# Performance work log

Hardware: AMD Instinct MI355X
Metric: run time of the kernel (lower is better)

The kernel has to match this reference:

```python
import jax, jax.numpy as jnp
import numpy as np

B, CIN, X, Y, Z = 4, 1, 64, 64, 64
W = 32          # fno_layer_size
L = 6           # num_fno_layers
M = 32          # modes per axis
CLIFT = CIN + 3 # coord features appended


def setup_inputs() -> dict:
    key = jax.random.key(0)
    ks = jax.random.split(key, 16)
    scale = 1.0 / (W * W)
    inp = {
        "x": jax.random.normal(ks[0], (B, CIN, X, Y, Z), dtype=jnp.float32),
        # lift network (two 1x1 conv3d layers)
        "lw1": jax.random.normal(ks[1], (W // 2, CLIFT), dtype=jnp.float32) * 0.1,
        "lb1": jnp.zeros((W // 2,), dtype=jnp.float32),
        "lw2": jax.random.normal(ks[2], (W, W // 2), dtype=jnp.float32) * 0.1,
        "lb2": jnp.zeros((W,), dtype=jnp.float32),
        # factorized spectral weights per layer: [L, in, out, modes, 2]
        "wx": jax.random.uniform(ks[3], (L, W, W, M, 2), dtype=jnp.float32) * scale,
        "wy": jax.random.uniform(ks[4], (L, W, W, M, 2), dtype=jnp.float32) * scale,
        "wz": jax.random.uniform(ks[5], (L, W, W, M, 2), dtype=jnp.float32) * scale,
        # per-layer MLP (1x1 conv3d: W -> 2W -> W)
        "mw1": jax.random.normal(ks[6], (L, 2 * W, W), dtype=jnp.float32) * 0.1,
        "mb1": jnp.zeros((L, 2 * W), dtype=jnp.float32),
        "mw2": jax.random.normal(ks[7], (L, W, 2 * W), dtype=jnp.float32) * 0.1,
        "mb2": jnp.zeros((L, W), dtype=jnp.float32),
    }
    return inp


def _pw(x, w, b):
    # 1x1x1 conv3d == per-voxel channel matmul
    return jnp.einsum('bixyz,oi->boxyz', x, w) + b[None, :, None, None, None]


def _spectral(x, wx, wy, wz):
    # x: [B, C, X, Y, Z]; wx/wy/wz: [C, C, M, 2] real -> complex
    cx = wx[..., 0] + 1j * wx[..., 1]
    cy = wy[..., 0] + 1j * wy[..., 1]
    cz = wz[..., 0] + 1j * wz[..., 1]
    _, _, sx, sy, sz = x.shape
    # z axis
    xf = jnp.fft.rfft(x, axis=-1, norm='ortho')
    oz = jnp.einsum('bixyz,ioz->boxyz', xf[..., :M], cz)
    oz = jnp.pad(oz, [(0, 0)] * 4 + [(0, sz // 2 + 1 - M)])
    out = jnp.fft.irfft(oz, n=sz, axis=-1, norm='ortho')
    # y axis
    xf = jnp.fft.rfft(x, axis=-2, norm='ortho')
    oy = jnp.einsum('bixyz,ioy->boxyz', xf[:, :, :, :M, :], cy)
    oy = jnp.pad(oy, [(0, 0)] * 3 + [(0, sy // 2 + 1 - M), (0, 0)])
    out = out + jnp.fft.irfft(oy, n=sy, axis=-2, norm='ortho')
    # x axis
    xf = jnp.fft.rfft(x, axis=-3, norm='ortho')
    ox = jnp.einsum('bixyz,iox->boxyz', xf[:, :, :M, :, :], cx)
    ox = jnp.pad(ox, [(0, 0)] * 2 + [(0, sx // 2 + 1 - M), (0, 0), (0, 0)])
    out = out + jnp.fft.irfft(ox, n=sx, axis=-3, norm='ortho')
    return out


def _meshgrid(b, sx, sy, sz, dtype):
    gx = jnp.linspace(0.0, 1.0, sx, dtype=dtype)
    gy = jnp.linspace(0.0, 1.0, sy, dtype=dtype)
    gz = jnp.linspace(0.0, 1.0, sz, dtype=dtype)
    GX, GY, GZ = jnp.meshgrid(gx, gy, gz, indexing='ij')
    g = jnp.stack([GX, GY, GZ], axis=0)            # [3, X, Y, Z]
    return jnp.broadcast_to(g[None], (b, 3, sx, sy, sz))


def reference(x, lw1, lb1, lw2, lb2, wx, wy, wz, mw1, mb1, mw2, mb2):
    b = x.shape[0]
    coord = _meshgrid(b, X, Y, Z, x.dtype)
    h = jnp.concatenate([x, coord], axis=1)         # [B, CIN+3, X, Y, Z]
    h = _pw(h, lw1, lb1)
    h = jax.nn.gelu(h, approximate=False)
    h = _pw(h, lw2, lb2)
    for l in range(L):
        s = _spectral(h, wx[l], wy[l], wz[l])
        s = _pw(s, mw1[l], mb1[l])
        s = jax.nn.gelu(s, approximate=False)
        s = _pw(s, mw2[l], mb2[l])
        h = s + h
    return h
```

## Files before the change

kernel.cpp:

```cpp
#include <hip/hip_runtime.h>
#include <math.h>


#define BB 4
#define CC 32
#define NN 64
#define MM 32
#define NSITE 8
#define STH 512

__global__ __launch_bounds__(256) void lift_kernel(
    const float* __restrict__ x,
    const float* __restrict__ lw1, const float* __restrict__ lb1,
    const float* __restrict__ lw2, const float* __restrict__ lb2,
    float* __restrict__ h)
{
    __shared__ float w1[64], b1s[16], w2[512], b2s[32];
    int tid = threadIdx.x;
    if (tid < 64) w1[tid] = lw1[tid];
    if (tid < 16) b1s[tid] = lb1[tid];
    for (int i = tid; i < 512; i += 256) w2[i] = lw2[i];
    if (tid < 32) b2s[tid] = lb2[tid];
    __syncthreads();

    int v = blockIdx.x * 256 + tid;
    int b = v >> 18;
    int vox = v & 262143;
    float feat0 = x[b * 262144 + vox];
    float feat1 = (float)(vox >> 12)        * (1.0f / 63.0f);
    float feat2 = (float)((vox >> 6) & 63)  * (1.0f / 63.0f);
    float feat3 = (float)(vox & 63)         * (1.0f / 63.0f);

    float t1[16];
#pragma unroll
    for (int o = 0; o < 16; ++o) {
        float a = b1s[o];
        a = fmaf(w1[o * 4 + 0], feat0, a);
        a = fmaf(w1[o * 4 + 1], feat1, a);
        a = fmaf(w1[o * 4 + 2], feat2, a);
        a = fmaf(w1[o * 4 + 3], feat3, a);
        t1[o] = 0.5f * a * (1.0f + erff(a * 0.70710678118654752f));
    }
    int base = b * CC * 262144 + vox;
#pragma unroll
    for (int c = 0; c < 32; ++c) {
        float a = b2s[c];
#pragma unroll
        for (int o = 0; o < 16; ++o) a = fmaf(w2[c * 16 + o], t1[o], a);
        h[base + c * 262144] = a;
    }
}

template <int AXIS, bool ACCUM>
__global__ __launch_bounds__(STH) void spectral_kernel(
    const float* __restrict__ h, float* __restrict__ sout,
    const float2* __restrict__ w)
{
    __shared__ float lds[34176];
    float*  xm    = lds;
    float2* mspec = (float2*)lds;
    float2* spec  = (float2*)(lds + 16896);
    float*  ybuf  = lds + 16896;
    float2* roots = (float2*)(lds + 34048);

    const int tid = threadIdx.x;
    const int site0 = blockIdx.x * NSITE;
    const int b  = site0 >> 12;
    const int q0 = site0 & 4095;

    if (tid < 64) {
        float ss, sc;
        sincosf((float)tid * (6.283185307179586f / 64.0f), &ss, &sc);
        roots[tid] = make_float2(sc, ss);
    }
    __syncthreads();

#pragma unroll
    for (int k = 0; k < 32; ++k) {
        int e = tid + k * STH;
        int c, s, t;
        if (AXIS == 2) { t = e & 63; s = (e >> 6) & 7; c = e >> 9; }
        else           { s = e & 7;  t = (e >> 3) & 63; c = e >> 9; }
        int q = q0 + s;
        int addr;
        if (AXIS == 2)      addr = (b * CC + c) * 262144 + q * 64 + t;
        else if (AXIS == 1) addr = (b * CC + c) * 262144 + (q >> 6) * 4096 + t * 64 + (q & 63);
        else                addr = (b * CC + c) * 262144 + t * 4096 + (q >> 6) * 64 + (q & 63);
        xm[(c * NSITE + s) * 66 + t] = h[addr];
    }
    __syncthreads();

    {
        const int mt = tid & 7;
        const int lt = tid >> 3;
        const int m0 = mt * 4;
        float ar[4][4], ai[4][4];
#pragma unroll
        for (int j = 0; j < 4; ++j)
#pragma unroll
            for (int i = 0; i < 4; ++i) { ar[j][i] = 0.0f; ai[j][i] = 0.0f; }
        int idx0 = 0, idx1 = 0, idx2 = 0, idx3 = 0;
        for (int t = 0; t < 64; ++t) {
            float xv[4];
#pragma unroll
            for (int j = 0; j < 4; ++j) xv[j] = xm[(lt * 4 + j) * 66 + t];
            float2 r0 = roots[idx0], r1 = roots[idx1], r2 = roots[idx2], r3 = roots[idx3];
            idx0 = (idx0 + m0 + 0) & 63;
            idx1 = (idx1 + m0 + 1) & 63;
            idx2 = (idx2 + m0 + 2) & 63;
            idx3 = (idx3 + m0 + 3) & 63;
#pragma unroll
            for (int j = 0; j < 4; ++j) {
                ar[j][0] = fmaf(xv[j], r0.x, ar[j][0]); ai[j][0] = fmaf(-xv[j], r0.y, ai[j][0]);
                ar[j][1] = fmaf(xv[j], r1.x, ar[j][1]); ai[j][1] = fmaf(-xv[j], r1.y, ai[j][1]);
                ar[j][2] = fmaf(xv[j], r2.x, ar[j][2]); ai[j][2] = fmaf(-xv[j], r2.y, ai[j][2]);
                ar[j][3] = fmaf(xv[j], r3.x, ar[j][3]); ai[j][3] = fmaf(-xv[j], r3.y, ai[j][3]);
            }
        }
#pragma unroll
        for (int j = 0; j < 4; ++j) {
            int line = lt * 4 + j;
            int c = line >> 3, s = line & 7;
#pragma unroll
            for (int i = 0; i < 4; ++i)
                spec[(s * CC + c) * MM + m0 + i] =
                    make_float2(ar[j][i] * 0.125f, ai[j][i] * 0.125f);
        }
    }
    __syncthreads();

    {
        const int m  = tid & 31;
        const int st = (tid >> 5) & 1;
        const int ot = tid >> 6;
        float ar[4][4], ai[4][4];
#pragma unroll
        for (int js = 0; js < 4; ++js)
#pragma unroll
            for (int jo = 0; jo < 4; ++jo) { ar[js][jo] = 0.0f; ai[js][jo] = 0.0f; }
        for (int i = 0; i < CC; ++i) {
            float2 sv[4];
#pragma unroll
            for (int js = 0; js < 4; ++js) sv[js] = spec[((st * 4 + js) * CC + i) * MM + m];
#pragma unroll
            for (int jo = 0; jo < 4; ++jo) {
                float2 wv = w[(i * CC + ot * 4 + jo) * MM + m];
#pragma unroll
                for (int js = 0; js < 4; ++js) {
                    ar[js][jo] = fmaf(sv[js].x, wv.x, fmaf(-sv[js].y, wv.y, ar[js][jo]));
                    ai[js][jo] = fmaf(sv[js].x, wv.y, fmaf( sv[js].y, wv.x, ai[js][jo]));
                }
            }
        }
        __syncthreads();
#pragma unroll
        for (int js = 0; js < 4; ++js) {
            int s = st * 4 + js;
#pragma unroll
            for (int jo = 0; jo < 4; ++jo) {
                int o = ot * 4 + jo;
                mspec[(o * NSITE + s) * 33 + m] = make_float2(ar[js][jo], ai[js][jo]);
            }
        }
    }
    __syncthreads();

    {
        const int tt = tid & 7;
        const int lt = tid >> 3;
        float acc[4][8];
#pragma unroll
        for (int j = 0; j < 4; ++j) {
            float m0r = mspec[(lt * 4 + j) * 33].x;
#pragma unroll
            for (int u = 0; u < 8; ++u) acc[j][u] = 0.5f * m0r;
        }
        for (int m = 1; m < 32; ++m) {
            float2 sv[4];
#pragma unroll
            for (int j = 0; j < 4; ++j) sv[j] = mspec[(lt * 4 + j) * 33 + m];
            int idx = (m * tt * 8) & 63;
#pragma unroll
            for (int u = 0; u < 8; ++u) {
                float2 rt = roots[idx];
                idx = (idx + m) & 63;
#pragma unroll
                for (int j = 0; j < 4; ++j) {
                    acc[j][u] = fmaf(sv[j].x, rt.x, acc[j][u]);
                    acc[j][u] = fmaf(-sv[j].y, rt.y, acc[j][u]);
                }
            }
        }
#pragma unroll
        for (int j = 0; j < 4; ++j)
#pragma unroll
            for (int u = 0; u < 8; ++u)
                ybuf[(lt * 4 + j) * 67 + tt * 8 + u] = acc[j][u] * 0.25f;
    }
    __syncthreads();

#pragma unroll
    for (int k = 0; k < 32; ++k) {
        int e = tid + k * STH;
        int o, s, t;
        if (AXIS == 2) { t = e & 63; s = (e >> 6) & 7; o = e >> 9; }
        else           { s = e & 7;  t = (e >> 3) & 63; o = e >> 9; }
        int q = q0 + s;
        int addr;
        if (AXIS == 2)      addr = (b * CC + o) * 262144 + q * 64 + t;
        else if (AXIS == 1) addr = (b * CC + o) * 262144 + (q >> 6) * 4096 + t * 64 + (q & 63);
        else                addr = (b * CC + o) * 262144 + t * 4096 + (q >> 6) * 64 + (q & 63);
        float v = ybuf[(o * NSITE + s) * 67 + t];
        if (ACCUM) sout[addr] += v;
        else       sout[addr] = v;
    }
}

__global__ __launch_bounds__(256) void mlp_kernel(
    const float* __restrict__ sin_, float* hio,
    const float* __restrict__ mw1, const float* __restrict__ mb1,
    const float* __restrict__ mw2, const float* __restrict__ mb2)
{
    __shared__ float w1[2048], bb1[64], w2[2048], bb2[32];
    int tid = threadIdx.x;
    for (int i = tid; i < 2048; i += 256) { w1[i] = mw1[i]; w2[i] = mw2[i]; }
    if (tid < 64) bb1[tid] = mb1[tid];
    if (tid < 32) bb2[tid] = mb2[tid];
    __syncthreads();

    int v = blockIdx.x * 256 + tid;
    int b = v >> 18;
    int vox = v & 262143;
    int base = b * CC * 262144 + vox;

    float sv[32];
#pragma unroll
    for (int i = 0; i < 32; ++i) sv[i] = sin_[base + i * 262144];

    float t1[64];
#pragma unroll
    for (int o = 0; o < 64; ++o) {
        float a = bb1[o];
#pragma unroll
        for (int i = 0; i < 32; ++i) a = fmaf(w1[o * 32 + i], sv[i], a);
        t1[o] = 0.5f * a * (1.0f + erff(a * 0.70710678118654752f));
    }
#pragma unroll
    for (int c = 0; c < 32; ++c) {
        float a = bb2[c];
#pragma unroll
        for (int o = 0; o < 64; ++o) a = fmaf(w2[c * 64 + o], t1[o], a);
        hio[base + c * 262144] += a;
    }
}

extern "C" void kernel_launch(void* const* d_in, const int* in_sizes, int n_in,
                              void* d_out, int out_size, void* d_ws, size_t ws_size,
                              hipStream_t stream) {
    const float* x   = (const float*)d_in[0];
    const float* lw1 = (const float*)d_in[1];
    const float* lb1 = (const float*)d_in[2];
    const float* lw2 = (const float*)d_in[3];
    const float* lb2 = (const float*)d_in[4];
    const float* wx  = (const float*)d_in[5];
    const float* wy  = (const float*)d_in[6];
    const float* wz  = (const float*)d_in[7];
    const float* mw1 = (const float*)d_in[8];
    const float* mb1 = (const float*)d_in[9];
    const float* mw2 = (const float*)d_in[10];
    const float* mb2 = (const float*)d_in[11];

    float* h = (float*)d_out;
    float* s = (float*)d_ws;

    lift_kernel<<<4096, 256, 0, stream>>>(x, lw1, lb1, lw2, lb2, h);

    for (int l = 0; l < 6; ++l) {
        const float2* wxl = (const float2*)wx + l * 32768;
        const float2* wyl = (const float2*)wy + l * 32768;
        const float2* wzl = (const float2*)wz + l * 32768;
        spectral_kernel<2, false><<<2048, STH, 0, stream>>>(h, s, wzl);
        spectral_kernel<1, true ><<<2048, STH, 0, stream>>>(h, s, wyl);
        spectral_kernel<0, true ><<<2048, STH, 0, stream>>>(h, s, wxl);
        mlp_kernel<<<4096, 256, 0, stream>>>(s, h,
            mw1 + l * 2048, mb1 + l * 64, mw2 + l * 2048, mb2 + l * 32);
    }
}
```

Before: 9.702 ms.

## Halve spectral sites per block and restructure MLP for fewer live registers

The spectral kernel now handles 4 lines per block instead of 8. This halves its LDS footprint and per-thread accumulator arrays and doubles the grid, with a launch-bounds hint asking for 4 blocks per CU, so more blocks fit on each CU. The MLP kernel no longer holds a 64-wide hidden vector in registers. It processes the hidden layer in chunks of 16 and accumulates outputs directly, reading a transposed second weight matrix from LDS as float4. The trade-off is less reuse per block in the spectral stages, since each thread covers fewer lines per twiddle or weight load, and possible spills if the register bounds are too tight.

Measured after the change: 32.23 ms. 3.32x slower.

```diff
diff --git a/kernel.cpp b/kernel.cpp
--- a/kernel.cpp
+++ b/kernel.cpp
@@ -6,7 +6,7 @@
 #define CC 32
 #define NN 64
 #define MM 32
-#define NSITE 8
+#define NSITE 4
 #define STH 512
 
 __global__ __launch_bounds__(256) void lift_kernel(
@@ -52,16 +52,16 @@
 }
 
 template <int AXIS, bool ACCUM>
-__global__ __launch_bounds__(STH) void spectral_kernel(
+__global__ __launch_bounds__(STH, 4) void spectral_kernel(
     const float* __restrict__ h, float* __restrict__ sout,
     const float2* __restrict__ w)
 {
-    __shared__ float lds[34176];
+    __shared__ float lds[17152];
     float*  xm    = lds;
     float2* mspec = (float2*)lds;
-    float2* spec  = (float2*)(lds + 16896);
-    float*  ybuf  = lds + 16896;
-    float2* roots = (float2*)(lds + 34048);
+    float2* spec  = (float2*)(lds + 8448);
+    float*  ybuf  = lds + 8448;
+    float2* roots = (float2*)(lds + 17024);
 
     const int tid = threadIdx.x;
     const int site0 = blockIdx.x * NSITE;
@@ -73,14 +73,13 @@
         sincosf((float)tid * (6.283185307179586f / 64.0f), &ss, &sc);
         roots[tid] = make_float2(sc, ss);
     }
-    __syncthreads();
-
-#pragma unroll
-    for (int k = 0; k < 32; ++k) {
+
+#pragma unroll
+    for (int k = 0; k < 16; ++k) {
         int e = tid + k * STH;
         int c, s, t;
-        if (AXIS == 2) { t = e & 63; s = (e >> 6) & 7; c = e >> 9; }
-        else           { s = e & 7;  t = (e >> 3) & 63; c = e >> 9; }
+        if (AXIS == 2) { t = e & 63; s = (e >> 6) & 3; c = e >> 8; }
+        else           { s = e & 3;  t = (e >> 2) & 63; c = e >> 8; }
         int q = q0 + s;
         int addr;
         if (AXIS == 2)      addr = (b * CC + c) * 262144 + q * 64 + t;
@@ -94,23 +93,23 @@
         const int mt = tid & 7;
         const int lt = tid >> 3;
         const int m0 = mt * 4;
-        float ar[4][4], ai[4][4];
-#pragma unroll
-        for (int j = 0; j < 4; ++j)
+        float ar[2][4], ai[2][4];
+#pragma unroll
+        for (int j = 0; j < 2; ++j)
 #pragma unroll
             for (int i = 0; i < 4; ++i) { ar[j][i] = 0.0f; ai[j][i] = 0.0f; }
         int idx0 = 0, idx1 = 0, idx2 = 0, idx3 = 0;
         for (int t = 0; t < 64; ++t) {
-            float xv[4];
-#pragma unroll
-            for (int j = 0; j < 4; ++j) xv[j] = xm[(lt * 4 + j) * 66 + t];
+            float xv[2];
+#pragma unroll
+            for (int j = 0; j < 2; ++j) xv[j] = xm[(lt * 2 + j) * 66 + t];
             float2 r0 = roots[idx0], r1 = roots[idx1], r2 = roots[idx2], r3 = roots[idx3];
             idx0 = (idx0 + m0 + 0) & 63;
             idx1 = (idx1 + m0 + 1) & 63;
             idx2 = (idx2 + m0 + 2) & 63;
             idx3 = (idx3 + m0 + 3) & 63;
 #pragma unroll
-            for (int j = 0; j < 4; ++j) {
+            for (int j = 0; j < 2; ++j) {
                 ar[j][0] = fmaf(xv[j], r0.x, ar[j][0]); ai[j][0] = fmaf(-xv[j], r0.y, ai[j][0]);
                 ar[j][1] = fmaf(xv[j], r1.x, ar[j][1]); ai[j][1] = fmaf(-xv[j], r1.y, ai[j][1]);
                 ar[j][2] = fmaf(xv[j], r2.x, ar[j][2]); ai[j][2] = fmaf(-xv[j], r2.y, ai[j][2]);
@@ -118,9 +117,9 @@
             }
         }
 #pragma unroll
-        for (int j = 0; j < 4; ++j) {
-            int line = lt * 4 + j;
-            int c = line >> 3, s = line & 7;
+        for (int j = 0; j < 2; ++j) {
+            int line = lt * 2 + j;
+            int c = line >> 2, s = line & 3;
 #pragma unroll
             for (int i = 0; i < 4; ++i)
                 spec[(s * CC + c) * MM + m0 + i] =
@@ -131,22 +130,22 @@
 
     {
         const int m  = tid & 31;
-        const int st = (tid >> 5) & 1;
+        const int sp = (tid >> 5) & 1;
         const int ot = tid >> 6;
-        float ar[4][4], ai[4][4];
-#pragma unroll
-        for (int js = 0; js < 4; ++js)
+        float ar[2][4], ai[2][4];
+#pragma unroll
+        for (int js = 0; js < 2; ++js)
 #pragma unroll
             for (int jo = 0; jo < 4; ++jo) { ar[js][jo] = 0.0f; ai[js][jo] = 0.0f; }
         for (int i = 0; i < CC; ++i) {
-            float2 sv[4];
-#pragma unroll
-            for (int js = 0; js < 4; ++js) sv[js] = spec[((st * 4 + js) * CC + i) * MM + m];
+            float2 sv[2];
+#pragma unroll
+            for (int js = 0; js < 2; ++js) sv[js] = spec[((sp * 2 + js) * CC + i) * MM + m];
 #pragma unroll
             for (int jo = 0; jo < 4; ++jo) {
                 float2 wv = w[(i * CC + ot * 4 + jo) * MM + m];
 #pragma unroll
-                for (int js = 0; js < 4; ++js) {
+                for (int js = 0; js < 2; ++js) {
                     ar[js][jo] = fmaf(sv[js].x, wv.x, fmaf(-sv[js].y, wv.y, ar[js][jo]));
                     ai[js][jo] = fmaf(sv[js].x, wv.y, fmaf( sv[js].y, wv.x, ai[js][jo]));
                 }
@@ -154,8 +153,8 @@
         }
         __syncthreads();
 #pragma unroll
-        for (int js = 0; js < 4; ++js) {
-            int s = st * 4 + js;
+        for (int js = 0; js < 2; ++js) {
+            int s = sp * 2 + js;
 #pragma unroll
             for (int jo = 0; jo < 4; ++jo) {
                 int o = ot * 4 + jo;
@@ -168,43 +167,43 @@
     {
         const int tt = tid & 7;
         const int lt = tid >> 3;
-        float acc[4][8];
-#pragma unroll
-        for (int j = 0; j < 4; ++j) {
-            float m0r = mspec[(lt * 4 + j) * 33].x;
+        float acc[2][8];
+#pragma unroll
+        for (int j = 0; j < 2; ++j) {
+            float m0r = mspec[(lt * 2 + j) * 33].x;
 #pragma unroll
             for (int u = 0; u < 8; ++u) acc[j][u] = 0.5f * m0r;
         }
         for (int m = 1; m < 32; ++m) {
-            float2 sv[4];
-#pragma unroll
-            for (int j = 0; j < 4; ++j) sv[j] = mspec[(lt * 4 + j) * 33 + m];
+            float2 sv[2];
+#pragma unroll
+            for (int j = 0; j < 2; ++j) sv[j] = mspec[(lt * 2 + j) * 33 + m];
             int idx = (m * tt * 8) & 63;
 #pragma unroll
             for (int u = 0; u < 8; ++u) {
                 float2 rt = roots[idx];
                 idx = (idx + m) & 63;
 #pragma unroll
-                for (int j = 0; j < 4; ++j) {
+                for (int j = 0; j < 2; ++j) {
                     acc[j][u] = fmaf(sv[j].x, rt.x, acc[j][u]);
                     acc[j][u] = fmaf(-sv[j].y, rt.y, acc[j][u]);
                 }
             }
         }
 #pragma unroll
-        for (int j = 0; j < 4; ++j)
+        for (int j = 0; j < 2; ++j)
 #pragma unroll
             for (int u = 0; u < 8; ++u)
-                ybuf[(lt * 4 + j) * 67 + tt * 8 + u] = acc[j][u] * 0.25f;
-    }
-    __syncthreads();
-
-#pragma unroll
-    for (int k = 0; k < 32; ++k) {
+                ybuf[(lt * 2 + j) * 67 + tt * 8 + u] = acc[j][u] * 0.25f;
+    }
+    __syncthreads();
+
+#pragma unroll
+    for (int k = 0; k < 16; ++k) {
         int e = tid + k * STH;
         int o, s, t;
-        if (AXIS == 2) { t = e & 63; s = (e >> 6) & 7; o = e >> 9; }
-        else           { s = e & 7;  t = (e >> 3) & 63; o = e >> 9; }
+        if (AXIS == 2) { t = e & 63; s = (e >> 6) & 3; o = e >> 8; }
+        else           { s = e & 3;  t = (e >> 2) & 63; o = e >> 8; }
         int q = q0 + s;
         int addr;
         if (AXIS == 2)      addr = (b * CC + o) * 262144 + q * 64 + t;
@@ -216,17 +215,27 @@
     }
 }
 
-__global__ __launch_bounds__(256) void mlp_kernel(
+__global__ __launch_bounds__(256, 4) void mlp_kernel(
     const float* __restrict__ sin_, float* hio,
     const float* __restrict__ mw1, const float* __restrict__ mb1,
     const float* __restrict__ mw2, const float* __restrict__ mb2)
 {
-    __shared__ float w1[2048], bb1[64], w2[2048], bb2[32];
+    __shared__ float w1[2048];
+    __shared__ float w2t[2048];
+    __shared__ float bb1[64], bb2[32];
     int tid = threadIdx.x;
-    for (int i = tid; i < 2048; i += 256) { w1[i] = mw1[i]; w2[i] = mw2[i]; }
+#pragma unroll
+    for (int k = 0; k < 8; ++k) {
+        int i = tid + k * 256;
+        w1[i] = mw1[i];
+        w2t[(i & 63) * 32 + (i >> 6)] = mw2[i];
+    }
     if (tid < 64) bb1[tid] = mb1[tid];
     if (tid < 32) bb2[tid] = mb2[tid];
     __syncthreads();
+
+    const float4* w1v  = (const float4*)w1;
+    const float4* w2tv = (const float4*)w2t;
 
     int v = blockIdx.x * 256 + tid;
     int b = v >> 18;
@@ -237,21 +246,43 @@
 #pragma unroll
     for (int i = 0; i < 32; ++i) sv[i] = sin_[base + i * 262144];
 
-    float t1[64];
-#pragma unroll
-    for (int o = 0; o < 64; ++o) {
-        float a = bb1[o];
-#pragma unroll
-        for (int i = 0; i < 32; ++i) a = fmaf(w1[o * 32 + i], sv[i], a);
-        t1[o] = 0.5f * a * (1.0f + erff(a * 0.70710678118654752f));
-    }
-#pragma unroll
-    for (int c = 0; c < 32; ++c) {
-        float a = bb2[c];
-#pragma unroll
-        for (int o = 0; o < 64; ++o) a = fmaf(w2[c * 64 + o], t1[o], a);
-        hio[base + c * 262144] += a;
-    }
+    float acc[32];
+#pragma unroll
+    for (int c = 0; c < 32; ++c) acc[c] = bb2[c];
+
+#pragma unroll
+    for (int ch = 0; ch < 4; ++ch) {
+        float t1c[16];
+#pragma unroll
+        for (int o16 = 0; o16 < 16; ++o16) {
+            int o = ch * 16 + o16;
+            float a = bb1[o];
+#pragma unroll
+            for (int i4 = 0; i4 < 8; ++i4) {
+                float4 wv = w1v[o * 8 + i4];
+                a = fmaf(wv.x, sv[i4 * 4 + 0], a);
+                a = fmaf(wv.y, sv[i4 * 4 + 1], a);
+                a = fmaf(wv.z, sv[i4 * 4 + 2], a);
+                a = fmaf(wv.w, sv[i4 * 4 + 3], a);
+            }
+            t1c[o16] = 0.5f * a * (1.0f + erff(a * 0.70710678118654752f));
+        }
+#pragma unroll
+        for (int o16 = 0; o16 < 16; ++o16) {
+            int o = ch * 16 + o16;
+            float tv = t1c[o16];
+#pragma unroll
+            for (int c4 = 0; c4 < 8; ++c4) {
+                float4 wv = w2tv[o * 8 + c4];
+                acc[c4 * 4 + 0] = fmaf(wv.x, tv, acc[c4 * 4 + 0]);
+                acc[c4 * 4 + 1] = fmaf(wv.y, tv, acc[c4 * 4 + 1]);
+                acc[c4 * 4 + 2] = fmaf(wv.z, tv, acc[c4 * 4 + 2]);
+                acc[c4 * 4 + 3] = fmaf(wv.w, tv, acc[c4 * 4 + 3]);
+            }
+        }
+    }
+#pragma unroll
+    for (int c = 0; c < 32; ++c) hio[base + c * 262144] += acc[c];
 }
 
 extern "C" void kernel_launch(void* const* d_in, const int* in_sizes, int n_in,
@@ -279,9 +310,9 @@
         const float2* wxl = (const float2*)wx + l * 32768;
         const float2* wyl = (const float2*)wy + l * 32768;
         const float2* wzl = (const float2*)wz + l * 32768;
-        spectral_kernel<2, false><<<2048, STH, 0, stream>>>(h, s, wzl);
-        spectral_kernel<1, true ><<<2048, STH, 0, stream>>>(h, s, wyl);
-        spectral_kernel<0, true ><<<2048, STH, 0, stream>>>(h, s, wxl);
+        spectral_kernel<2, false><<<4096, STH, 0, stream>>>(h, s, wzl);
+        spectral_kernel<1, true ><<<4096, STH, 0, stream>>>(h, s, wyl);
+        spectral_kernel<0, true ><<<4096, STH, 0, stream>>>(h, s, wxl);
         mlp_kernel<<<4096, 256, 0, stream>>>(s, h,
             mw1 + l * 2048, mb1 + l * 64, mw2 + l * 2048, mb2 + l * 32);
     }
```

## Exploit real-input DFT symmetry in spectral kernel and stream MLP weights from global

Applied to the files above, without the earlier changes.

The forward DFT now pairs samples t and 64-t, so each cosine and sine multiply covers two inputs and the loop runs about half as many iterations. The inverse DFT uses the matching symmetry to produce outputs p and 64-p from one pair of accumulations, cutting its FLOPs roughly in half. The MLP kernel drops its LDS weight staging and reads uniform float4 weights straight from global memory, and interleaves the two layers in chunks of 16 to limit register pressure. One __syncthreads after the root-table setup is removed, which is only safe because the barrier after the loads still orders the roots before they are read.

Result: slower. 10.51 ms (+8.3%).

```diff
diff --git a/kernel.cpp b/kernel.cpp
--- a/kernel.cpp
+++ b/kernel.cpp
@@ -73,7 +73,6 @@
         sincosf((float)tid * (6.283185307179586f / 64.0f), &ss, &sc);
         roots[tid] = make_float2(sc, ss);
     }
-    __syncthreads();
 
 #pragma unroll
     for (int k = 0; k < 32; ++k) {
@@ -96,14 +95,25 @@
         const int m0 = mt * 4;
         float ar[4][4], ai[4][4];
 #pragma unroll
-        for (int j = 0; j < 4; ++j)
-#pragma unroll
-            for (int i = 0; i < 4; ++i) { ar[j][i] = 0.0f; ai[j][i] = 0.0f; }
-        int idx0 = 0, idx1 = 0, idx2 = 0, idx3 = 0;
-        for (int t = 0; t < 64; ++t) {
-            float xv[4];
-#pragma unroll
-            for (int j = 0; j < 4; ++j) xv[j] = xm[(lt * 4 + j) * 66 + t];
+        for (int j = 0; j < 4; ++j) {
+            float x0  = xm[(lt * 4 + j) * 66 + 0];
+            float x32 = xm[(lt * 4 + j) * 66 + 32];
+#pragma unroll
+            for (int i = 0; i < 4; ++i) {
+                ar[j][i] = (i & 1) ? (x0 - x32) : (x0 + x32);
+                ai[j][i] = 0.0f;
+            }
+        }
+        int idx0 = m0 + 0, idx1 = m0 + 1, idx2 = m0 + 2, idx3 = m0 + 3;
+        for (int t = 1; t < 32; ++t) {
+            float p[4], q[4];
+#pragma unroll
+            for (int j = 0; j < 4; ++j) {
+                float xa = xm[(lt * 4 + j) * 66 + t];
+                float xb = xm[(lt * 4 + j) * 66 + 64 - t];
+                p[j] = xa + xb;
+                q[j] = xa - xb;
+            }
             float2 r0 = roots[idx0], r1 = roots[idx1], r2 = roots[idx2], r3 = roots[idx3];
             idx0 = (idx0 + m0 + 0) & 63;
             idx1 = (idx1 + m0 + 1) & 63;
@@ -111,10 +121,10 @@
             idx3 = (idx3 + m0 + 3) & 63;
 #pragma unroll
             for (int j = 0; j < 4; ++j) {
-                ar[j][0] = fmaf(xv[j], r0.x, ar[j][0]); ai[j][0] = fmaf(-xv[j], r0.y, ai[j][0]);
-                ar[j][1] = fmaf(xv[j], r1.x, ar[j][1]); ai[j][1] = fmaf(-xv[j], r1.y, ai[j][1]);
-                ar[j][2] = fmaf(xv[j], r2.x, ar[j][2]); ai[j][2] = fmaf(-xv[j], r2.y, ai[j][2]);
-                ar[j][3] = fmaf(xv[j], r3.x, ar[j][3]); ai[j][3] = fmaf(-xv[j], r3.y, ai[j][3]);
+                ar[j][0] = fmaf(p[j], r0.x, ar[j][0]); ai[j][0] = fmaf(-q[j], r0.y, ai[j][0]);
+                ar[j][1] = fmaf(p[j], r1.x, ar[j][1]); ai[j][1] = fmaf(-q[j], r1.y, ai[j][1]);
+                ar[j][2] = fmaf(p[j], r2.x, ar[j][2]); ai[j][2] = fmaf(-q[j], r2.y, ai[j][2]);
+                ar[j][3] = fmaf(p[j], r3.x, ar[j][3]); ai[j][3] = fmaf(-q[j], r3.y, ai[j][3]);
             }
         }
 #pragma unroll
@@ -168,34 +178,48 @@
     {
         const int tt = tid & 7;
         const int lt = tid >> 3;
-        float acc[4][8];
+        float u[4][4], vv[4][4], wsum[4], m0r[4];
 #pragma unroll
         for (int j = 0; j < 4; ++j) {
-            float m0r = mspec[(lt * 4 + j) * 33].x;
-#pragma unroll
-            for (int u = 0; u < 8; ++u) acc[j][u] = 0.5f * m0r;
-        }
+            m0r[j] = mspec[(lt * 4 + j) * 33].x;
+            wsum[j] = 0.0f;
+#pragma unroll
+            for (int jj = 0; jj < 4; ++jj) { u[j][jj] = 0.5f * m0r[j]; vv[j][jj] = 0.0f; }
+        }
+        const int p0 = tt * 4 + 1, p1 = tt * 4 + 2, p2 = tt * 4 + 3, p3 = tt * 4 + 4;
+        int i0 = p0, i1 = p1, i2 = p2, i3 = p3;
         for (int m = 1; m < 32; ++m) {
             float2 sv[4];
 #pragma unroll
             for (int j = 0; j < 4; ++j) sv[j] = mspec[(lt * 4 + j) * 33 + m];
-            int idx = (m * tt * 8) & 63;
-#pragma unroll
-            for (int u = 0; u < 8; ++u) {
-                float2 rt = roots[idx];
-                idx = (idx + m) & 63;
-#pragma unroll
-                for (int j = 0; j < 4; ++j) {
-                    acc[j][u] = fmaf(sv[j].x, rt.x, acc[j][u]);
-                    acc[j][u] = fmaf(-sv[j].y, rt.y, acc[j][u]);
-                }
-            }
-        }
-#pragma unroll
-        for (int j = 0; j < 4; ++j)
-#pragma unroll
-            for (int u = 0; u < 8; ++u)
-                ybuf[(lt * 4 + j) * 67 + tt * 8 + u] = acc[j][u] * 0.25f;
+            float2 r0 = roots[i0], r1 = roots[i1], r2 = roots[i2], r3 = roots[i3];
+            i0 = (i0 + p0) & 63;
+            i1 = (i1 + p1) & 63;
+            i2 = (i2 + p2) & 63;
+            i3 = (i3 + p3) & 63;
+#pragma unroll
+            for (int j = 0; j < 4; ++j) {
+                u[j][0] = fmaf(sv[j].x, r0.x, u[j][0]); vv[j][0] = fmaf(sv[j].y, r0.y, vv[j][0]);
+                u[j][1] = fmaf(sv[j].x, r1.x, u[j][1]); vv[j][1] = fmaf(sv[j].y, r1.y, vv[j][1]);
+                u[j][2] = fmaf(sv[j].x, r2.x, u[j][2]); vv[j][2] = fmaf(sv[j].y, r2.y, vv[j][2]);
+                u[j][3] = fmaf(sv[j].x, r3.x, u[j][3]); vv[j][3] = fmaf(sv[j].y, r3.y, vv[j][3]);
+                wsum[j] += sv[j].x;
+            }
+        }
+#pragma unroll
+        for (int j = 0; j < 4; ++j) {
+            int line = lt * 4 + j;
+            ybuf[line * 67 + p0]               = (u[j][0] - vv[j][0]) * 0.25f;
+            ybuf[line * 67 + ((64 - p0) & 63)] = (u[j][0] + vv[j][0]) * 0.25f;
+            ybuf[line * 67 + p1]               = (u[j][1] - vv[j][1]) * 0.25f;
+            ybuf[line * 67 + ((64 - p1) & 63)] = (u[j][1] + vv[j][1]) * 0.25f;
+            ybuf[line * 67 + p2]               = (u[j][2] - vv[j][2]) * 0.25f;
+            ybuf[line * 67 + ((64 - p2) & 63)] = (u[j][2] + vv[j][2]) * 0.25f;
+            ybuf[line * 67 + p3]               = (u[j][3] - vv[j][3]) * 0.25f;
+            ybuf[line * 67 + ((64 - p3) & 63)] = (u[j][3] + vv[j][3]) * 0.25f;
+            if (tt == 0)
+                ybuf[line * 67 + 0] = (0.5f * m0r[j] + wsum[j]) * 0.25f;
+        }
     }
     __syncthreads();
 
@@ -217,17 +241,14 @@
 }
 
 __global__ __launch_bounds__(256) void mlp_kernel(
-    const float* __restrict__ sin_, float* hio,
+    const float* __restrict__ sin_, float* __restrict__ hio,
     const float* __restrict__ mw1, const float* __restrict__ mb1,
     const float* __restrict__ mw2, const float* __restrict__ mb2)
 {
-    __shared__ float w1[2048], bb1[64], w2[2048], bb2[32];
+    const float4* w1v = (const float4*)mw1;
+    const float4* w2v = (const float4*)mw2;
+
     int tid = threadIdx.x;
-    for (int i = tid; i < 2048; i += 256) { w1[i] = mw1[i]; w2[i] = mw2[i]; }
-    if (tid < 64) bb1[tid] = mb1[tid];
-    if (tid < 32) bb2[tid] = mb2[tid];
-    __syncthreads();
-
     int v = blockIdx.x * 256 + tid;
     int b = v >> 18;
     int vox = v & 262143;
@@ -237,21 +258,41 @@
 #pragma unroll
     for (int i = 0; i < 32; ++i) sv[i] = sin_[base + i * 262144];
 
-    float t1[64];
-#pragma unroll
-    for (int o = 0; o < 64; ++o) {
-        float a = bb1[o];
-#pragma unroll
-        for (int i = 0; i < 32; ++i) a = fmaf(w1[o * 32 + i], sv[i], a);
-        t1[o] = 0.5f * a * (1.0f + erff(a * 0.70710678118654752f));
-    }
-#pragma unroll
-    for (int c = 0; c < 32; ++c) {
-        float a = bb2[c];
-#pragma unroll
-        for (int o = 0; o < 64; ++o) a = fmaf(w2[c * 64 + o], t1[o], a);
-        hio[base + c * 262144] += a;
-    }
+    float acc[32];
+#pragma unroll
+    for (int c = 0; c < 32; ++c) acc[c] = mb2[c];
+
+#pragma unroll
+    for (int ch = 0; ch < 4; ++ch) {
+        float t1c[16];
+#pragma unroll
+        for (int o16 = 0; o16 < 16; ++o16) {
+            int o = ch * 16 + o16;
+            float a = mb1[o];
+#pragma unroll
+            for (int i4 = 0; i4 < 8; ++i4) {
+                float4 wv = w1v[o * 8 + i4];
+                a = fmaf(wv.x, sv[i4 * 4 + 0], a);
+                a = fmaf(wv.y, sv[i4 * 4 + 1], a);
+                a = fmaf(wv.z, sv[i4 * 4 + 2], a);
+                a = fmaf(wv.w, sv[i4 * 4 + 3], a);
+            }
+            t1c[o16] = 0.5f * a * (1.0f + erff(a * 0.70710678118654752f));
+        }
+#pragma unroll
+        for (int c = 0; c < 32; ++c) {
+#pragma unroll
+            for (int o4 = 0; o4 < 4; ++o4) {
+                float4 wv = w2v[c * 16 + ch * 4 + o4];
+                acc[c] = fmaf(wv.x, t1c[o4 * 4 + 0], acc[c]);
+                acc[c] = fmaf(wv.y, t1c[o4 * 4 + 1], acc[c]);
+                acc[c] = fmaf(wv.z, t1c[o4 * 4 + 2], acc[c]);
+                acc[c] = fmaf(wv.w, t1c[o4 * 4 + 3], acc[c]);
+            }
+        }
+    }
+#pragma unroll
+    for (int c = 0; c < 32; ++c) hio[base + c * 262144] += acc[c];
 }
 
 extern "C" void kernel_launch(void* const* d_in, const int* in_sizes, int n_in,
```
